# Optimization experiments

Hardware: AMD Instinct MI355X
Metric: run time of the kernel (lower is better)

## Reference

```python
import jax, jax.numpy as jnp
import numpy as np

S, B, E, D, H, F, L = 1024, 8, 768, 8, 8, 2048, 4
D = 1024  # HIDDEN_DIM
H = 8     # nhead
DH = D // H
EPS = 1e-5


def _ln(x, g, b):
    m = jnp.mean(x, -1, keepdims=True)
    v = jnp.mean(jnp.square(x - m), -1, keepdims=True)
    return (x - m) * jax.lax.rsqrt(v + EPS) * g + b


def setup_inputs() -> dict:
    key = jax.random.key(0)
    ks = iter(jax.random.split(key, 16))
    n = lambda shape: jax.random.normal(next(ks), shape, jnp.float32) * 0.02
    return dict(
        x=jax.random.normal(next(ks), (S, B, E), jnp.float32),
        enc_w=n((D, E)), enc_b=jnp.zeros((D,), jnp.float32),
        enc_ln_g=jnp.ones((D,), jnp.float32), enc_ln_b=jnp.zeros((D,), jnp.float32),
        qkv_w=n((L, 3 * D, D)), qkv_b=jnp.zeros((L, 3 * D), jnp.float32),
        out_w=n((L, D, D)), out_b=jnp.zeros((L, D), jnp.float32),
        ln1_g=jnp.ones((L, D), jnp.float32), ln1_b=jnp.zeros((L, D), jnp.float32),
        ff1_w=n((L, F, D)), ff1_b=jnp.zeros((L, F), jnp.float32),
        ff2_w=n((L, D, F)), ff2_b=jnp.zeros((L, D), jnp.float32),
        ln2_g=jnp.ones((L, D), jnp.float32), ln2_b=jnp.zeros((L, D), jnp.float32),
        dec_w1=n((D // 2, D)), dec_b1=jnp.zeros((D // 2,), jnp.float32),
        dec_ln_g=jnp.ones((D // 2,), jnp.float32), dec_ln_b=jnp.zeros((D // 2,), jnp.float32),
        dec_w2=n((E, D // 2)), dec_b2=jnp.zeros((E,), jnp.float32),
    )


def reference(x, enc_w, enc_b, enc_ln_g, enc_ln_b, qkv_w, qkv_b, out_w, out_b,
              ln1_g, ln1_b, ff1_w, ff1_b, ff2_w, ff2_b, ln2_g, ln2_b,
              dec_w1, dec_b1, dec_ln_g, dec_ln_b, dec_w2, dec_b2):
    # encoder MLP: Linear -> LayerNorm -> ReLU (dropout = identity at eval)
    h = jax.nn.relu(_ln(x @ enc_w.T + enc_b, enc_ln_g, enc_ln_b))  # (S,B,D)
    scale = np.float32(1.0 / np.sqrt(DH))
    for l in range(L):  # 4 post-norm TransformerEncoderLayers, eager attention
        qkv = h @ qkv_w[l].T + qkv_b[l]                    # (S,B,3D)
        q, k, v = jnp.split(qkv, 3, axis=-1)
        q = q.reshape(S, B, H, DH)
        k = k.reshape(S, B, H, DH)
        v = v.reshape(S, B, H, DH)
        scores = jnp.einsum('sbhd,tbhd->bhst', q, k) * scale  # (B,H,S,S)
        p = jax.nn.softmax(scores, axis=-1)
        o = jnp.einsum('bhst,tbhd->sbhd', p, v).reshape(S, B, D)
        o = o @ out_w[l].T + out_b[l]
        h = _ln(h + o, ln1_g[l], ln1_b[l])
        f = jax.nn.relu(h @ ff1_w[l].T + ff1_b[l]) @ ff2_w[l].T + ff2_b[l]
        h = _ln(h + f, ln2_g[l], ln2_b[l])
    # decoder MLP
    d = jax.nn.relu(_ln(h @ dec_w1.T + dec_b1, dec_ln_g, dec_ln_b))
    return d @ dec_w2.T + dec_b2  # (S,B,E)
```

## Files before the change

kernel.cpp:

```cpp
#include <hip/hip_runtime.h>
#include <math.h>

#define S_ 1024
#define B_ 8
#define E_ 768
#define D_ 1024
#define H_ 8
#define F_ 2048
#define L_ 4
#define M_ (S_*B_)

typedef unsigned short u16;
typedef unsigned int u32;
typedef u16 u16x8 __attribute__((ext_vector_type(8)));
typedef u16 u16x4 __attribute__((ext_vector_type(4)));
typedef u16 u16x2 __attribute__((ext_vector_type(2)));
typedef u32 u32x2 __attribute__((ext_vector_type(2)));
typedef short bf16x8 __attribute__((ext_vector_type(8)));
typedef float f32x4 __attribute__((ext_vector_type(4)));

#define AS1 __attribute__((address_space(1)))
#define AS3 __attribute__((address_space(3)))

#define QSCALE 0.127517432f

__device__ __forceinline__ void gload_lds16(const void* g, void* l) {
  __builtin_amdgcn_global_load_lds((const AS1 void*)g, (AS3 void*)l, 16, 0, 0);
}
__device__ __forceinline__ u16 f2bf(float f) {
  unsigned u = __builtin_bit_cast(unsigned, f);
  return (u16)((u + 0x7fffu + ((u >> 16) & 1u)) >> 16);
}
__device__ __forceinline__ float bf2f(u16 h) {
  unsigned u = ((unsigned)h) << 16;
  return __builtin_bit_cast(float, u);
}
__device__ __forceinline__ u32 cvtpk(float a, float b) {
  u32 r;
  asm("v_cvt_pk_bf16_f32 %0, %1, %2" : "=v"(r) : "v"(a), "v"(b));
  return r;
}

__global__ __launch_bounds__(256) void conv4(
    const float* __restrict__ s0, u16* __restrict__ d0, int n0,
    const float* __restrict__ s1, u16* __restrict__ d1, int n1,
    const float* __restrict__ s2, u16* __restrict__ d2, int n2,
    const float* __restrict__ s3, u16* __restrict__ d3, int n3)
{
  int total = (n0 + n1 + n2 + n3) >> 2;
  for (int i = blockIdx.x * 256 + threadIdx.x; i < total; i += gridDim.x * 256) {
    int e = i << 2;
    const float* s; u16* d; int off;
    if (e < n0)           { s = s0; d = d0; off = e; }
    else if (e < n0+n1)   { s = s1; d = d1; off = e - n0; }
    else if (e < n0+n1+n2){ s = s2; d = d2; off = e - n0 - n1; }
    else                  { s = s3; d = d3; off = e - n0 - n1 - n2; }
    float4 v = *(const float4*)&s[off];
    u16x4 o; o[0]=f2bf(v.x); o[1]=f2bf(v.y); o[2]=f2bf(v.z); o[3]=f2bf(v.w);
    *(u16x4*)&d[off] = o;
  }
}

template<int ACT, int OUTBF, int SCQ>
__global__ __launch_bounds__(512) void gemm256(
    const u16* __restrict__ A, const u16* __restrict__ W,
    const float* __restrict__ bias, void* __restrict__ Cout,
    int M, int N, int K)
{
  __shared__ u16 lds[49152];
  const int gx = gridDim.x, nwg = gx * gridDim.y;
  const int lin = blockIdx.y * gx + blockIdx.x;
  const int work = (lin & 7) * (nwg >> 3) + (lin >> 3);
  const int bm = (work / gx) * 256, bn = (work % gx) * 128;
  const int tid = threadIdx.x;
  const int l = tid & 63;
  const int w = tid >> 6;
  const int l15 = l & 15, lg = l >> 4;
  const int wr = w >> 2, wc = w & 3;
  const int srow = tid >> 3;
  const int scb  = tid & 7;

  f32x4 acc[8][2] = {};

  const int nt = K >> 6;

#define STAGE(c, k0)                                                        \
  {                                                                         \
    u16* Ab = lds + (c)*16384;                                              \
    u16* Bb = lds + 32768 + (c)*8192;                                       \
    _Pragma("unroll")                                                       \
    for (int u = 0; u < 4; ++u) {                                           \
      int row = u*64 + srow;                                                \
      int cb  = scb ^ (row & 7);                                            \
      gload_lds16(A + (size_t)(bm + row) * K + (k0) + cb*8,                 \
                  Ab + u*4096 + tid*8);                                     \
    }                                                                       \
    _Pragma("unroll")                                                       \
    for (int u = 0; u < 2; ++u) {                                           \
      int row = u*64 + srow;                                                \
      int cb  = scb ^ (row & 7);                                            \
      gload_lds16(W + (size_t)(bn + row) * K + (k0) + cb*8,                 \
                  Bb + u*4096 + tid*8);                                     \
    }                                                                       \
  }

  STAGE(0, 0);
  __syncthreads();

  for (int t = 0; t < nt; ++t) {
    int c = t & 1;
    if (t + 1 < nt) STAGE(c ^ 1, (t + 1) << 6);
    const u16* Ab = lds + c*16384;
    const u16* Bb = lds + 32768 + c*8192;
    #pragma unroll
    for (int ks = 0; ks < 2; ++ks) {
      bf16x8 af[8], bf_[2];
      #pragma unroll
      for (int mi = 0; mi < 8; ++mi) {
        int row = wr*128 + mi*16 + l15;
        af[mi] = *(const bf16x8*)&Ab[row*64 + ((ks*4 + lg) ^ (row & 7))*8];
      }
      #pragma unroll
      for (int ni = 0; ni < 2; ++ni) {
        int row = wc*32 + ni*16 + l15;
        bf_[ni] = *(const bf16x8*)&Bb[row*64 + ((ks*4 + lg) ^ (row & 7))*8];
      }
      #pragma unroll
      for (int mi = 0; mi < 8; ++mi)
        #pragma unroll
        for (int ni = 0; ni < 2; ++ni)
          acc[mi][ni] = __builtin_amdgcn_mfma_f32_16x16x32_bf16(af[mi], bf_[ni], acc[mi][ni], 0, 0, 0);
    }
    __syncthreads();
  }
#undef STAGE

  u16* Cb = (u16*)Cout; float* Cf = (float*)Cout;
  #pragma unroll
  for (int ni = 0; ni < 2; ++ni) {
    int col = bn + wc*32 + ni*16 + l15;
    float bv = bias[col];
    #pragma unroll
    for (int mi = 0; mi < 8; ++mi) {
      #pragma unroll
      for (int rr = 0; rr < 4; ++rr) {
        int row = bm + wr*128 + mi*16 + lg*4 + rr;
        float v = acc[mi][ni][rr] + bv;
        if (ACT) v = fmaxf(v, 0.f);
        if (SCQ) { if (col < 1024) v *= QSCALE; }
        if (OUTBF) Cb[(size_t)row * N + col] = f2bf(v);
        else       Cf[(size_t)row * N + col] = v;
      }
    }
  }
}

template<int ACT, int OUTBF, int SCQ>
__global__ __launch_bounds__(256) void gemm_mfma(
    const u16* __restrict__ A, const u16* __restrict__ W,
    const float* __restrict__ bias, void* __restrict__ Cout,
    int M, int N, int K)
{
  __shared__ u16 As[128*32];
  __shared__ u16 Bs[128*32];
  const int gx = gridDim.x, nwg = gx * gridDim.y;
  const int lin = blockIdx.y * gx + blockIdx.x;
  const int work = (lin & 7) * (nwg >> 3) + (lin >> 3);
  const int bm = (work / gx) * 128, bn = (work % gx) * 128;
  const int tid = threadIdx.x;
  const int w = tid >> 6, l = tid & 63;
  const int l15 = l & 15, lg = l >> 4;
  const int wr = w >> 1, wc = w & 1;
  f32x4 acc[4][4] = {};

  for (int k0 = 0; k0 < K; k0 += 32) {
    __syncthreads();
    #pragma unroll
    for (int j = 0; j < 2; ++j) {
      int e = (w*2 + j) * 512 + l * 8;
      int row = e >> 5, ko = (l & 3) * 8;
      gload_lds16(A + (size_t)(bm + row) * K + k0 + ko, &As[(w*2 + j) * 512]);
      gload_lds16(W + (size_t)(bn + row) * K + k0 + ko, &Bs[(w*2 + j) * 512]);
    }
    __syncthreads();
    bf16x8 af[4], bf_[4];
    #pragma unroll
    for (int mi = 0; mi < 4; ++mi) {
      int row = wr*64 + mi*16 + l15;
      af[mi] = *(const bf16x8*)&As[row*32 + lg*8];
    }
    #pragma unroll
    for (int ni = 0; ni < 4; ++ni) {
      int row = wc*64 + ni*16 + l15;
      bf_[ni] = *(const bf16x8*)&Bs[row*32 + lg*8];
    }
    #pragma unroll
    for (int mi = 0; mi < 4; ++mi)
      #pragma unroll
      for (int ni = 0; ni < 4; ++ni)
        acc[mi][ni] = __builtin_amdgcn_mfma_f32_16x16x32_bf16(af[mi], bf_[ni], acc[mi][ni], 0, 0, 0);
  }

  u16* Cb = (u16*)Cout; float* Cf = (float*)Cout;
  #pragma unroll
  for (int ni = 0; ni < 4; ++ni) {
    int col = bn + wc*64 + ni*16 + l15;
    float bv = bias[col];
    #pragma unroll
    for (int mi = 0; mi < 4; ++mi) {
      #pragma unroll
      for (int rr = 0; rr < 4; ++rr) {
        int row = bm + wr*64 + mi*16 + lg*4 + rr;
        float v = acc[mi][ni][rr] + bv;
        if (ACT) v = fmaxf(v, 0.f);
        if (SCQ) { if (col < 1024) v *= QSCALE; }
        if (OUTBF) Cb[(size_t)row * N + col] = f2bf(v);
        else       Cf[(size_t)row * N + col] = v;
      }
    }
  }
}

template<int NV, bool RESID, bool RELU>
__global__ __launch_bounds__(256) void ln_bf16(
    const u16* __restrict__ X, const u16* __restrict__ R,
    const float* __restrict__ g, const float* __restrict__ b,
    u16* __restrict__ Y)
{
  constexpr int D = NV * 256;
  __shared__ float sbuf[8];
  const int tid = threadIdx.x;
  const size_t base = (size_t)blockIdx.x * D + tid * NV;
  float v[NV];
  if constexpr (NV == 4) {
    u16x4 xv = *(const u16x4*)&X[base];
    #pragma unroll
    for (int i = 0; i < 4; ++i) v[i] = bf2f(xv[i]);
    if (RESID) {
      u16x4 rv = *(const u16x4*)&R[base];
      #pragma unroll
      for (int i = 0; i < 4; ++i) v[i] += bf2f(rv[i]);
    }
  } else {
    u16x2 xv = *(const u16x2*)&X[base];
    #pragma unroll
    for (int i = 0; i < 2; ++i) v[i] = bf2f(xv[i]);
    if (RESID) {
      u16x2 rv = *(const u16x2*)&R[base];
      #pragma unroll
      for (int i = 0; i < 2; ++i) v[i] += bf2f(rv[i]);
    }
  }
  float sum = 0.f, sq = 0.f;
  #pragma unroll
  for (int i = 0; i < NV; ++i) { sum += v[i]; sq += v[i]*v[i]; }
  #pragma unroll
  for (int off = 32; off > 0; off >>= 1) {
    sum += __shfl_down(sum, off);
    sq  += __shfl_down(sq, off);
  }
  if ((tid & 63) == 0) { sbuf[tid >> 6] = sum; sbuf[4 + (tid >> 6)] = sq; }
  __syncthreads();
  sum = sbuf[0] + sbuf[1] + sbuf[2] + sbuf[3];
  sq  = sbuf[4] + sbuf[5] + sbuf[6] + sbuf[7];
  const float mean = sum / (float)D;
  const float rstd = rsqrtf(sq / (float)D - mean*mean + 1e-5f);
  const int c0 = tid * NV;
  if constexpr (NV == 4) {
    u16x4 o;
    #pragma unroll
    for (int i = 0; i < 4; ++i) {
      float t = (v[i] - mean) * rstd * g[c0+i] + b[c0+i];
      if (RELU) t = fmaxf(t, 0.f);
      o[i] = f2bf(t);
    }
    *(u16x4*)&Y[base] = o;
  } else {
    u16x2 o;
    #pragma unroll
    for (int i = 0; i < 2; ++i) {
      float t = (v[i] - mean) * rstd * g[c0+i] + b[c0+i];
      if (RELU) t = fmaxf(t, 0.f);
      o[i] = f2bf(t);
    }
    *(u16x2*)&Y[base] = o;
  }
}

__global__ __launch_bounds__(256) void vtrans(
    const u16* __restrict__ QKV, u16* __restrict__ Vt)
{
  __shared__ u16 Ls[32*132];
  const int st = blockIdx.x, bh = blockIdx.y;
  const int bb = bh >> 3, hh = bh & 7;
  const int t = threadIdx.x;
  #pragma unroll
  for (int i = 0; i < 2; ++i) {
    int e = i*256 + t;
    int s = e >> 4, d0 = (e & 15) * 8;
    u16x8 v = *(const u16x8*)&QKV[(size_t)((st*32 + s)*8 + bb)*3072 + 2048 + hh*128 + d0];
    #pragma unroll
    for (int j = 0; j < 4; ++j) {
      u16x2 p; p[0] = v[2*j]; p[1] = v[2*j+1];
      *(u16x2*)&Ls[s*132 + d0 + 2*j] = p;
    }
  }
  __syncthreads();
  #pragma unroll
  for (int i = 0; i < 2; ++i) {
    int e = i*256 + t;
    int d = e >> 2, s0 = (e & 3) * 8;
    u16x8 v;
    #pragma unroll
    for (int j = 0; j < 8; ++j) v[j] = Ls[(s0+j)*132 + d];
    *(u16x8*)&Vt[(size_t)bh*131072 + (size_t)d*1024 + st*32 + s0] = v;
  }
}

__global__ __launch_bounds__(256) void attn_mfma(
    const u16* __restrict__ QKV, const u16* __restrict__ Vt,
    u16* __restrict__ AO)
{
  __shared__ u16 Ks[64*128];
  __shared__ u16 Vs[128*64];
  __shared__ u16 Pl[4][16*64];
  const int bid = blockIdx.x;
  const int wg = (bid & 7) * 128 + (bid >> 3);
  const int qt = wg & 15, bh = wg >> 4;
  const int bb = bh >> 3, hh = bh & 7;
  const int tid = threadIdx.x, w = tid >> 6, l = tid & 63;
  const int l15 = l & 15, lg = l >> 4;

  bf16x8 aq[4];
  {
    int q = qt*64 + w*16 + l15;
    const u16* qp = QKV + (size_t)(q*8 + bb)*3072 + hh*128 + lg*8;
    #pragma unroll
    for (int kc = 0; kc < 4; ++kc)
      aq[kc] = *(const bf16x8*)(qp + kc*32);
  }
  const u16* vbase = Vt + (size_t)bh*131072;

  f32x4 of[8] = {};
  float mreg = -INFINITY, lpart = 0.f;
  const int psw = (l15 & 7) << 3;

  for (int kt = 0; kt < 16; ++kt) {
    __syncthreads();
    #pragma unroll
    for (int i = 0; i < 4; ++i) {
      int e = (w*4 + i) * 512 + l * 8;
      int krow = e >> 7, d0 = e & 127;
      int dsw = d0 ^ ((krow & 7) << 3);
      gload_lds16(QKV + (size_t)((kt*64 + krow)*8 + bb)*3072 + 1024 + hh*128 + dsw,
                  &Ks[(w*4 + i) * 512]);
      int vd = e >> 6, vc = e & 63;
      int vsw = vc ^ ((vd & 7) << 3);
      gload_lds16(vbase + (size_t)vd*1024 + kt*64 + vsw,
                  &Vs[(w*4 + i) * 512]);
    }
    __syncthreads();

    f32x4 sf[4] = {};
    #pragma unroll
    for (int kc = 0; kc < 4; ++kc) {
      #pragma unroll
      for (int f = 0; f < 4; ++f) {
        int krow = f*16 + l15;
        bf16x8 bk = *(const bf16x8*)&Ks[krow*128 + ((kc*32 + lg*8) ^ ((krow & 7) << 3))];
        sf[f] = __builtin_amdgcn_mfma_f32_16x16x32_bf16(bk, aq[kc], sf[f], 0, 0, 0);
      }
    }

    float pm01 = fmaxf(fmaxf(sf[0][0], sf[0][1]), fmaxf(sf[0][2], sf[0][3]));
    float pm23 = fmaxf(fmaxf(sf[1][0], sf[1][1]), fmaxf(sf[1][2], sf[1][3]));
    float pm45 = fmaxf(fmaxf(sf[2][0], sf[2][1]), fmaxf(sf[2][2], sf[2][3]));
    float pm67 = fmaxf(fmaxf(sf[3][0], sf[3][1]), fmaxf(sf[3][2], sf[3][3]));
    float pmax = fmaxf(fmaxf(pm01, pm23), fmaxf(pm45, pm67));
    pmax = fmaxf(pmax, __shfl_xor(pmax, 16));
    pmax = fmaxf(pmax, __shfl_xor(pmax, 32));

    if (__any(pmax > mreg + 8.f)) {
      float mn = fmaxf(mreg, pmax);
      float al = exp2f(mreg - mn);
      mreg = mn;
      lpart *= al;
      #pragma unroll
      for (int r = 0; r < 4; ++r) {
        float alq = __shfl(al, (l & 48) + lg*4 + r);
        #pragma unroll
        for (int ni = 0; ni < 8; ++ni) of[ni][r] *= alq;
      }
    }

    float psum = 0.f;
    #pragma unroll
    for (int f = 0; f < 4; ++f) {
      float p0 = exp2f(sf[f][0] - mreg);
      float p1 = exp2f(sf[f][1] - mreg);
      float p2 = exp2f(sf[f][2] - mreg);
      float p3 = exp2f(sf[f][3] - mreg);
      psum += (p0 + p1) + (p2 + p3);
      u32x2 pk; pk[0] = cvtpk(p0, p1); pk[1] = cvtpk(p2, p3);
      *(u32x2*)&Pl[w][l15*64 + ((f*16 + lg*4) ^ psw)] = pk;
    }
    lpart += psum;

    bf16x8 pa0 = *(const bf16x8*)&Pl[w][l15*64 + ((lg*8) ^ psw)];
    bf16x8 pa1 = *(const bf16x8*)&Pl[w][l15*64 + ((32 + lg*8) ^ psw)];
    #pragma unroll
    for (int ni = 0; ni < 8; ++ni) {
      int n = ni*16 + l15;
      int nsw = (n & 7) << 3;
      bf16x8 vb0 = *(const bf16x8*)&Vs[n*64 + ((lg*8) ^ nsw)];
      bf16x8 vb1 = *(const bf16x8*)&Vs[n*64 + ((32 + lg*8) ^ nsw)];
      of[ni] = __builtin_amdgcn_mfma_f32_16x16x32_bf16(pa0, vb0, of[ni], 0, 0, 0);
      of[ni] = __builtin_amdgcn_mfma_f32_16x16x32_bf16(pa1, vb1, of[ni], 0, 0, 0);
    }
  }

  float ls = lpart;
  ls += __shfl_xor(ls, 16);
  ls += __shfl_xor(ls, 32);
  float inv = 1.f / ls;
  #pragma unroll
  for (int r = 0; r < 4; ++r) {
    float invq = __shfl(inv, (l & 48) + lg*4 + r);
    int q = qt*64 + w*16 + lg*4 + r;
    size_t base = (size_t)(q*8 + bb) * 1024 + hh*128;
    #pragma unroll
    for (int ni = 0; ni < 8; ++ni)
      AO[base + ni*16 + l15] = f2bf(of[ni][r] * invq);
  }
}

#define O_WENC  0ull
#define O_WDEC1 786432ull
#define O_WDEC2 1310720ull
#define O_WLQ   1703936ull
#define O_WLO   4849664ull
#define O_WLF1  5898240ull
#define O_WLF2  7995392ull
#define O_R     10092544ull
#define O_H     35258368ull
#define O_AO    43646976ull
#define O_VT    52035584ull

extern "C" void kernel_launch(void* const* d_in, const int* in_sizes, int n_in,
                              void* d_out, int out_size, void* d_ws, size_t ws_size,
                              hipStream_t stream) {
  (void)in_sizes; (void)n_in; (void)out_size; (void)ws_size;
  const float* x        = (const float*)d_in[0];
  const float* enc_w    = (const float*)d_in[1];
  const float* enc_b    = (const float*)d_in[2];
  const float* enc_ln_g = (const float*)d_in[3];
  const float* enc_ln_b = (const float*)d_in[4];
  const float* qkv_w    = (const float*)d_in[5];
  const float* qkv_b    = (const float*)d_in[6];
  const float* out_w    = (const float*)d_in[7];
  const float* out_b    = (const float*)d_in[8];
  const float* ln1_g    = (const float*)d_in[9];
  const float* ln1_b    = (const float*)d_in[10];
  const float* ff1_w    = (const float*)d_in[11];
  const float* ff1_b    = (const float*)d_in[12];
  const float* ff2_w    = (const float*)d_in[13];
  const float* ff2_b    = (const float*)d_in[14];
  const float* ln2_g    = (const float*)d_in[15];
  const float* ln2_b    = (const float*)d_in[16];
  const float* dec_w1   = (const float*)d_in[17];
  const float* dec_b1   = (const float*)d_in[18];
  const float* dec_ln_g = (const float*)d_in[19];
  const float* dec_ln_b = (const float*)d_in[20];
  const float* dec_w2   = (const float*)d_in[21];
  const float* dec_b2   = (const float*)d_in[22];

  u16* ws16 = (u16*)d_ws;
  u16* wenc  = ws16 + O_WENC;
  u16* wdec1 = ws16 + O_WDEC1;
  u16* wdec2 = ws16 + O_WDEC2;
  u16* wlq   = ws16 + O_WLQ;
  u16* wlo   = ws16 + O_WLO;
  u16* wlf1  = ws16 + O_WLF1;
  u16* wlf2  = ws16 + O_WLF2;
  u16* qkv   = ws16 + O_R;
  u16* bufY  = ws16 + O_R;
  u16* bufG  = ws16 + O_R + 8388608ull;
  u16* xb    = bufG;
  u16* dech  = bufG;
  u16* h     = ws16 + O_H;
  u16* ao    = ws16 + O_AO;
  u16* vt    = ws16 + O_VT;

  const dim3 blk(256);
  const dim3 blk5(512);

  conv4<<<1024, blk, 0, stream>>>(x, xb, 8192*768,
                                  enc_w, wenc, 1024*768,
                                  dec_w1, wdec1, 512*1024,
                                  dec_w2, wdec2, 768*512);
  gemm_mfma<0,1,0><<<dim3(8,64), blk, 0, stream>>>(xb, wenc, enc_b, bufY, M_, 1024, 768);
  ln_bf16<4,false,true><<<M_, blk, 0, stream>>>(bufY, nullptr, enc_ln_g, enc_ln_b, h);

  for (int l = 0; l < L_; ++l) {
    conv4<<<1024, blk, 0, stream>>>(qkv_w + (size_t)l*3145728, wlq, 3145728,
                                    out_w + (size_t)l*1048576, wlo, 1048576,
                                    ff1_w + (size_t)l*2097152, wlf1, 2097152,
                                    ff2_w + (size_t)l*2097152, wlf2, 2097152);
    gemm256<0,1,1><<<dim3(24,32), blk5, 0, stream>>>(h, wlq, qkv_b + (size_t)l*3072, qkv, M_, 3072, 1024);
    vtrans<<<dim3(32,64), blk, 0, stream>>>(qkv, vt);
    attn_mfma<<<1024, blk, 0, stream>>>(qkv, vt, ao);
    gemm256<0,1,0><<<dim3(8,32), blk5, 0, stream>>>(ao, wlo, out_b + (size_t)l*1024, bufY, M_, 1024, 1024);
    ln_bf16<4,true,false><<<M_, blk, 0, stream>>>(bufY, h, ln1_g + (size_t)l*1024, ln1_b + (size_t)l*1024, h);
    gemm256<1,1,0><<<dim3(16,32), blk5, 0, stream>>>(h, wlf1, ff1_b + (size_t)l*2048, bufG, M_, 2048, 1024);
    gemm256<0,1,0><<<dim3(8,32), blk5, 0, stream>>>(bufG, wlf2, ff2_b + (size_t)l*1024, bufY, M_, 1024, 2048);
    ln_bf16<4,true,false><<<M_, blk, 0, stream>>>(bufY, h, ln2_g + (size_t)l*1024, ln2_b + (size_t)l*1024, h);
  }

  gemm_mfma<0,1,0><<<dim3(4,64), blk, 0, stream>>>(h, wdec1, dec_b1, bufY, M_, 512, 1024);
  ln_bf16<2,false,true><<<M_, blk, 0, stream>>>(bufY, nullptr, dec_ln_g, dec_ln_b, dech);
  gemm_mfma<0,0,0><<<dim3(6,64), blk, 0, stream>>>(dech, wdec2, dec_b2, d_out, M_, 768, 512);
}
```

Before: 1.123 ms.

## Triple-buffer GEMM K loads and double-buffer attention KV tiles

The GEMM main loop moves from two LDS stages to three, issuing loads two tiles ahead and waiting with an explicit vmcnt count plus a raw barrier instead of a full __syncthreads each iteration. The attention kernel now uses 512-thread blocks covering 128 queries, so each K/V tile is shared by twice as many query rows, and it double-buffers K/V so the next tile loads while the current one is computed. The aim is to hide global-to-LDS latency and cut barrier stalls. The cost is more LDS per block (144KB for the GEMM), which may lower occupancy, and the hand-counted vmcnt waits must match the number of loads in flight.

```diff
diff --git a/kernel.cpp b/kernel.cpp
--- a/kernel.cpp
+++ b/kernel.cpp
@@ -67,7 +67,7 @@
     const float* __restrict__ bias, void* __restrict__ Cout,
     int M, int N, int K)
 {
-  __shared__ u16 lds[49152];
+  __shared__ u16 lds[73728];
   const int gx = gridDim.x, nwg = gx * gridDim.y;
   const int lin = blockIdx.y * gx + blockIdx.x;
   const int work = (lin & 7) * (nwg >> 3) + (lin >> 3);
@@ -81,13 +81,12 @@
   const int scb  = tid & 7;
 
   f32x4 acc[8][2] = {};
-
   const int nt = K >> 6;
 
 #define STAGE(c, k0)                                                        \
   {                                                                         \
-    u16* Ab = lds + (c)*16384;                                              \
-    u16* Bb = lds + 32768 + (c)*8192;                                       \
+    u16* Ab = lds + (c)*24576;                                              \
+    u16* Bb = Ab + 16384;                                                   \
     _Pragma("unroll")                                                       \
     for (int u = 0; u < 4; ++u) {                                           \
       int row = u*64 + srow;                                                \
@@ -105,13 +104,15 @@
   }
 
   STAGE(0, 0);
-  __syncthreads();
-
+  STAGE(1, 64);
+  asm volatile("s_waitcnt vmcnt(6)" ::: "memory");
+  __builtin_amdgcn_s_barrier();
+
+  int cr = 0, cw = 2;
   for (int t = 0; t < nt; ++t) {
-    int c = t & 1;
-    if (t + 1 < nt) STAGE(c ^ 1, (t + 1) << 6);
-    const u16* Ab = lds + c*16384;
-    const u16* Bb = lds + 32768 + c*8192;
+    if (t + 2 < nt) STAGE(cw, (t + 2) << 6);
+    const u16* Ab = lds + cr*24576;
+    const u16* Bb = Ab + 16384;
     #pragma unroll
     for (int ks = 0; ks < 2; ++ks) {
       bf16x8 af[8], bf_[2];
@@ -131,7 +132,13 @@
         for (int ni = 0; ni < 2; ++ni)
           acc[mi][ni] = __builtin_amdgcn_mfma_f32_16x16x32_bf16(af[mi], bf_[ni], acc[mi][ni], 0, 0, 0);
     }
-    __syncthreads();
+    if (t + 1 < nt) {
+      if (t + 2 < nt) { asm volatile("s_waitcnt vmcnt(6)" ::: "memory"); }
+      else            { asm volatile("s_waitcnt vmcnt(0)" ::: "memory"); }
+      __builtin_amdgcn_s_barrier();
+    }
+    cr = (cr == 2) ? 0 : cr + 1;
+    cw = (cw == 2) ? 0 : cw + 1;
   }
 #undef STAGE
 
@@ -317,49 +324,57 @@
   }
 }
 
-__global__ __launch_bounds__(256) void attn_mfma(
+__global__ __launch_bounds__(512, 4) void attn_mfma(
     const u16* __restrict__ QKV, const u16* __restrict__ Vt,
     u16* __restrict__ AO)
 {
-  __shared__ u16 Ks[64*128];
-  __shared__ u16 Vs[128*64];
-  __shared__ u16 Pl[4][16*64];
+  __shared__ u16 Ks[2][64*128];
+  __shared__ u16 Vs[2][128*64];
+  __shared__ u16 Pl[8][16*64];
   const int bid = blockIdx.x;
-  const int wg = (bid & 7) * 128 + (bid >> 3);
-  const int qt = wg & 15, bh = wg >> 4;
+  const int wg = (bid & 7) * 64 + (bid >> 3);
+  const int qt = wg & 7, bh = wg >> 3;
   const int bb = bh >> 3, hh = bh & 7;
   const int tid = threadIdx.x, w = tid >> 6, l = tid & 63;
   const int l15 = l & 15, lg = l >> 4;
 
   bf16x8 aq[4];
   {
-    int q = qt*64 + w*16 + l15;
+    int q = qt*128 + w*16 + l15;
     const u16* qp = QKV + (size_t)(q*8 + bb)*3072 + hh*128 + lg*8;
     #pragma unroll
     for (int kc = 0; kc < 4; ++kc)
       aq[kc] = *(const bf16x8*)(qp + kc*32);
   }
   const u16* vbase = Vt + (size_t)bh*131072;
+
+#define STAGE_KV(c, kt)                                                     \
+  {                                                                         \
+    _Pragma("unroll")                                                       \
+    for (int i = 0; i < 2; ++i) {                                           \
+      int e = (w*2 + i) * 512 + l * 8;                                      \
+      int krow = e >> 7, d0 = e & 127;                                      \
+      int dsw = d0 ^ ((krow & 7) << 3);                                     \
+      gload_lds16(QKV + (size_t)(((kt)*64 + krow)*8 + bb)*3072 + 1024       \
+                      + hh*128 + dsw,                                       \
+                  &Ks[c][(w*2 + i) * 512]);                                 \
+      int vd = e >> 6, vc = e & 63;                                         \
+      int vsw = vc ^ ((vd & 7) << 3);                                       \
+      gload_lds16(vbase + (size_t)vd*1024 + (kt)*64 + vsw,                  \
+                  &Vs[c][(w*2 + i) * 512]);                                 \
+    }                                                                       \
+  }
 
   f32x4 of[8] = {};
   float mreg = -INFINITY, lpart = 0.f;
   const int psw = (l15 & 7) << 3;
 
+  STAGE_KV(0, 0);
+  __syncthreads();
+
   for (int kt = 0; kt < 16; ++kt) {
-    __syncthreads();
-    #pragma unroll
-    for (int i = 0; i < 4; ++i) {
-      int e = (w*4 + i) * 512 + l * 8;
-      int krow = e >> 7, d0 = e & 127;
-      int dsw = d0 ^ ((krow & 7) << 3);
-      gload_lds16(QKV + (size_t)((kt*64 + krow)*8 + bb)*3072 + 1024 + hh*128 + dsw,
-                  &Ks[(w*4 + i) * 512]);
-      int vd = e >> 6, vc = e & 63;
-      int vsw = vc ^ ((vd & 7) << 3);
-      gload_lds16(vbase + (size_t)vd*1024 + kt*64 + vsw,
-                  &Vs[(w*4 + i) * 512]);
-    }
-    __syncthreads();
+    const int cur = kt & 1;
+    if (kt + 1 < 16) STAGE_KV(cur ^ 1, kt + 1);
 
     f32x4 sf[4] = {};
     #pragma unroll
@@ -367,7 +382,7 @@
       #pragma unroll
       for (int f = 0; f < 4; ++f) {
         int krow = f*16 + l15;
-        bf16x8 bk = *(const bf16x8*)&Ks[krow*128 + ((kc*32 + lg*8) ^ ((krow & 7) << 3))];
+        bf16x8 bk = *(const bf16x8*)&Ks[cur][krow*128 + ((kc*32 + lg*8) ^ ((krow & 7) << 3))];
         sf[f] = __builtin_amdgcn_mfma_f32_16x16x32_bf16(bk, aq[kc], sf[f], 0, 0, 0);
       }
     }
@@ -412,12 +427,15 @@
     for (int ni = 0; ni < 8; ++ni) {
       int n = ni*16 + l15;
       int nsw = (n & 7) << 3;
-      bf16x8 vb0 = *(const bf16x8*)&Vs[n*64 + ((lg*8) ^ nsw)];
-      bf16x8 vb1 = *(const bf16x8*)&Vs[n*64 + ((32 + lg*8) ^ nsw)];
+      bf16x8 vb0 = *(const bf16x8*)&Vs[cur][n*64 + ((lg*8) ^ nsw)];
+      bf16x8 vb1 = *(const bf16x8*)&Vs[cur][n*64 + ((32 + lg*8) ^ nsw)];
       of[ni] = __builtin_amdgcn_mfma_f32_16x16x32_bf16(pa0, vb0, of[ni], 0, 0, 0);
       of[ni] = __builtin_amdgcn_mfma_f32_16x16x32_bf16(pa1, vb1, of[ni], 0, 0, 0);
     }
-  }
+
+    if (kt + 1 < 16) __syncthreads();
+  }
+#undef STAGE_KV
 
   float ls = lpart;
   ls += __shfl_xor(ls, 16);
@@ -426,7 +444,7 @@
   #pragma unroll
   for (int r = 0; r < 4; ++r) {
     float invq = __shfl(inv, (l & 48) + lg*4 + r);
-    int q = qt*64 + w*16 + lg*4 + r;
+    int q = qt*128 + w*16 + lg*4 + r;
     size_t base = (size_t)(q*8 + bb) * 1024 + hh*128;
     #pragma unroll
     for (int ni = 0; ni < 8; ++ni)
@@ -508,7 +526,7 @@
                                     ff2_w + (size_t)l*2097152, wlf2, 2097152);
     gemm256<0,1,1><<<dim3(24,32), blk5, 0, stream>>>(h, wlq, qkv_b + (size_t)l*3072, qkv, M_, 3072, 1024);
     vtrans<<<dim3(32,64), blk, 0, stream>>>(qkv, vt);
-    attn_mfma<<<1024, blk, 0, stream>>>(qkv, vt, ao);
+    attn_mfma<<<512, blk5, 0, stream>>>(qkv, vt, ao);
     gemm256<0,1,0><<<dim3(8,32), blk5, 0, stream>>>(ao, wlo, out_b + (size_t)l*1024, bufY, M_, 1024, 1024);
     ln_bf16<4,true,false><<<M_, blk, 0, stream>>>(bufY, h, ln1_g + (size_t)l*1024, ln1_b + (size_t)l*1024, h);
     gemm256<1,1,0><<<dim3(16,32), blk5, 0, stream>>>(h, wlf1, ff1_b + (size_t)l*2048, bufG, M_, 2048, 1024);
```

Measured after the change: 1.064 ms. 1.06x faster.
